# Performance work log

Measured on AMD Instinct MI355X. Metric: run time of the kernel, lower is better.

The kernel has to match this reference:

```python
import math
import jax, jax.numpy as jnp
import numpy as np

COULOMB = 14.399645478425668  # eV*Angstrom / e^2


def setup_inputs() -> dict:
    key = jax.random.key(0)
    k0, k1, k2, k3, k4 = jax.random.split(key, 5)
    B, n, F, S = 128, 512, 64, 4  # molecules, atoms/molecule, feat dim, n species
    N = B * n
    node_features = jax.random.normal(k0, (N, F), dtype=jnp.float32)
    pos = jax.random.normal(k1, (N, 3), dtype=jnp.float32) * 5.0  # spread atoms out
    atom_type = jax.random.randint(k2, (N,), 0, S)
    total_charge = jnp.zeros((B, 1), dtype=jnp.float32)
    chi_weight = jax.random.normal(k3, (F, 1), dtype=jnp.float32) / np.float32(np.sqrt(F))
    hardness_param = jnp.ones((S,), dtype=jnp.float32)
    sigma = 0.3 + 0.5 * jax.random.uniform(k4, (S,), dtype=jnp.float32)  # covalent radii
    return dict(node_features=node_features, pos=pos, atom_type=atom_type,
                total_charge=total_charge, chi_weight=chi_weight,
                hardness_param=hardness_param, sigma=sigma, n_per_mol=n)


def reference(node_features, pos, atom_type, total_charge, chi_weight,
              hardness_param, sigma, n_per_mol):
    n = n_per_mol
    N, F = node_features.shape
    B = N // n

    feats = node_features.reshape(B, n, F)
    pos_b = pos.reshape(B, n, 3)
    sp = atom_type.reshape(B, n)

    chi = (feats @ chi_weight)[..., 0]                      # [B, n] electronegativity
    hard = jnp.square(hardness_param)[sp]                   # [B, n]
    sig = sigma[sp]                                         # [B, n]

    # pairwise distances within each molecule (diag masked for safe divide)
    diff = pos_b[:, :, None, :] - pos_b[:, None, :, :]      # [B, n, n, 3]
    d2 = jnp.sum(diff * diff, axis=-1)
    eye = jnp.eye(n, dtype=pos.dtype)
    d = jnp.sqrt(jnp.where(eye, 1.0, d2))                   # [B, n, n]

    gamma = jnp.sqrt(sig[:, :, None] ** 2 + sig[:, None, :] ** 2)
    off = COULOMB * jax.lax.erf(d / (math.sqrt(2.0) * gamma)) / d
    diag = hard + COULOMB / (math.sqrt(math.pi) * sig)      # [B, n]
    coeffs = off * (1.0 - eye) + eye * diag[:, :, None]     # [B, n, n]

    # augmented Qeq system with charge-conservation Lagrange multiplier
    A = jnp.ones((B, n + 1, n + 1), dtype=coeffs.dtype)
    A = A.at[:, :n, :n].set(coeffs)
    A = A.at[:, n, n].set(0.0)
    rhs = jnp.concatenate([-chi, total_charge], axis=1)     # [B, n+1]
    sol = jnp.linalg.solve(A, rhs[..., None])[..., 0]
    q = sol[:, :n]                                          # [B, n] charges

    # E = sum_{i<j} C_ij q_i q_j + sum_i (chi_i q_i + 0.5 diag_i q_i^2)
    #   = 0.5 q^T C q + chi . q   (C includes diagonal)
    e_qeq = 0.5 * jnp.einsum('bi,bij,bj->b', q, coeffs, q) + jnp.sum(chi * q, axis=1)
    return e_qeq[:, None], q.reshape(N, 1)
```

## Files before the change

kernel.cpp:

```cpp
#include <hip/hip_runtime.h>
#include <math.h>

#define NA 512
#define NN (NA*NA)
#define COULOMB 14.399645478425668f
#define SQRT_PI 1.7724538509055160273f

__device__ __forceinline__ float rl(float x, int lane) {
    return __int_as_float(__builtin_amdgcn_readlane(__float_as_int(x), lane));
}

__device__ __forceinline__ float pair_val(float dx, float dy, float dz,
                                          float s2i, float s2k) {
    float d2 = dx*dx + dy*dy + dz*dz;
    float rinv = rsqrtf(d2);
    return COULOMB * erff(d2 * rinv * rsqrtf(2.f * (s2i + s2k))) * rinv;
}

__global__ void k_pre(const float* __restrict__ feats, const float* __restrict__ w,
                      const int* __restrict__ type, const float* __restrict__ hard,
                      const float* __restrict__ sigma,
                      float* __restrict__ chi, float* __restrict__ diag,
                      float* __restrict__ sigA, int N) {
    __shared__ float wl[64];
    int tid = threadIdx.x;
    if (tid < 64) wl[tid] = w[tid];
    __syncthreads();
    int i = blockIdx.x * 256 + tid;
    if (i >= N) return;
    const float4* fp = (const float4*)(feats + (size_t)i * 64);
    float acc = 0.f;
#pragma unroll
    for (int q = 0; q < 16; q++) {
        float4 v = fp[q];
        acc += v.x * wl[4*q] + v.y * wl[4*q+1] + v.z * wl[4*q+2] + v.w * wl[4*q+3];
    }
    chi[i] = acc;
    int t = type[i];
    float s = sigma[t];
    float h = hard[t];
    sigA[i] = s;
    diag[i] = h * h + COULOMB / (SQRT_PI * s);
}

__global__ void __launch_bounds__(512, 2) k_panel(const float* __restrict__ pos,
                                                  const float* __restrict__ sigA,
                                                  const float* __restrict__ diagA,
                                                  float* __restrict__ C, const int j) {
    const int b = blockIdx.x;
    float* __restrict__ Cb = C + (size_t)b * NN;
    const int jb = j * 64;
    const int m = NA - jb - 64;
    const int tid = threadIdx.x;
    __shared__ float D[64 * 65];
    __shared__ float DT[64 * 64];
    __shared__ float invd[64];
    __shared__ float px[NA], py[NA], pz[NA], s2s[NA];

    if (j == 0) {
        if (tid < NA) {
            px[tid] = pos[((size_t)b * NA + tid) * 3 + 0];
            py[tid] = pos[((size_t)b * NA + tid) * 3 + 1];
            pz[tid] = pos[((size_t)b * NA + tid) * 3 + 2];
            float s = sigA[b * NA + tid];
            s2s[tid] = s * s;
        }
        __syncthreads();
    }

#pragma unroll
    for (int e = 0; e < 8; e++) {
        int f = e * 512 + tid;
        int rr = f >> 6, cc = f & 63;
        float v;
        if (j == 0) {
            if (rr == cc) v = diagA[b * NA + rr];
            else v = pair_val(px[rr]-px[cc], py[rr]-py[cc], pz[rr]-pz[cc], s2s[rr], s2s[cc]);
        } else {
            v = Cb[(size_t)(jb + rr) * NA + jb + cc];
        }
        D[rr * 65 + cc] = v;
    }

    float rv[64];
    const int r = tid - 64;
    if (r >= 0 && r < m) {
        const int g = jb + 64 + r;
        if (j == 0) {
#pragma unroll
            for (int k = 0; k < 64; k++)
                rv[k] = pair_val(px[g]-px[k], py[g]-py[k], pz[g]-pz[k], s2s[g], s2s[k]);
        } else {
            const float4* rp = (const float4*)(Cb + (size_t)g * NA + jb);
#pragma unroll
            for (int q = 0; q < 16; q++) {
                float4 v = rp[q];
                rv[4*q] = v.x; rv[4*q+1] = v.y; rv[4*q+2] = v.z; rv[4*q+3] = v.w;
            }
        }
    }
    __syncthreads();

    if (tid < 64) {
        const int t = tid;
        float cl[64];
#pragma unroll
        for (int i = 0; i < 64; i++) cl[i] = (i >= t) ? D[i * 65 + t] : D[t * 65 + i];
#pragma unroll
        for (int k = 0; k < 64; k++) {
            float pivot = rl(cl[k], k);
            float invp = 1.0f / pivot;
            float factor = (t > k) ? (cl[k] * invp) : 0.0f;
#pragma unroll
            for (int i = k + 1; i < 64; i++) {
                float bc = rl(cl[i], k);
                cl[i] -= bc * factor;
            }
        }
        float rs = 1.0f / sqrtf(cl[t]);
        invd[t] = rs;
#pragma unroll
        for (int i = 0; i < 64; i++)
            if (i >= t) D[i * 65 + t] = cl[i] * rs;
    }
    __syncthreads();

#pragma unroll
    for (int e = 0; e < 8; e++) {
        int f = e * 512 + tid;
        int row = f >> 6, cc = f & 63;
        float v = D[row * 65 + cc];
        DT[row * 64 + cc] = (cc < row) ? v : 0.f;
        if (cc <= row) Cb[(size_t)(jb + row) * NA + jb + cc] = v;
    }
    __syncthreads();

    if (r >= 0 && r < m) {
#pragma unroll
        for (int k = 0; k < 64; k++) {
            float acc = rv[k];
            const float4* Lr = (const float4*)(DT + k * 64);
            const int k4 = k >> 2;
#pragma unroll
            for (int t4 = 0; t4 < k4; t4++) {
                float4 Lv = Lr[t4];
                acc -= Lv.x * rv[4*t4] + Lv.y * rv[4*t4+1] + Lv.z * rv[4*t4+2] + Lv.w * rv[4*t4+3];
            }
#pragma unroll
            for (int tt = k4 * 4; tt < k; tt++) acc -= DT[k * 64 + tt] * rv[tt];
            rv[k] = acc * invd[k];
        }
        float4* rp = (float4*)(Cb + (size_t)(jb + 64 + r) * NA + jb);
#pragma unroll
        for (int q = 0; q < 16; q++)
            rp[q] = make_float4(rv[4*q], rv[4*q+1], rv[4*q+2], rv[4*q+3]);
    }
}

template<bool GEN>
__global__ void __launch_bounds__(256, 3) k_trail(float* __restrict__ C,
                                                  const float* __restrict__ pos,
                                                  const float* __restrict__ sigA,
                                                  const float* __restrict__ diagA,
                                                  const int j) {
    const int b = blockIdx.y;
    float* __restrict__ Cb = C + (size_t)b * NN;
    const int jb = j * 64;
    const int m = NA - jb - 64;
    int t = blockIdx.x;
    int RI = 0;
    while (t >= RI + 1) { t -= RI + 1; RI++; }
    const int RJ = t;
    const int RB = RI * 128, CB = RJ * 128;
    const int vr = min(128, m - RB);
    const int vc = min(128, m - CB);
    const int tid = threadIdx.x;
    const int rg = tid >> 4, cg = tid & 15;

    __shared__ float As[128 * 65];
    __shared__ float Bs[128 * 65];

    float acc[8][8];

    if (GEN) {
        __shared__ float pAx[128], pAy[128], pAz[128], sA[128], dA[128];
        __shared__ float pBx[128], pBy[128], pBz[128], sB[128];
        if (tid < 128) {
            if (RB + tid < m) {
                int ga = b * NA + jb + 64 + RB + tid;
                pAx[tid] = pos[(size_t)ga * 3 + 0];
                pAy[tid] = pos[(size_t)ga * 3 + 1];
                pAz[tid] = pos[(size_t)ga * 3 + 2];
                float s = sigA[ga]; sA[tid] = s * s;
                dA[tid] = diagA[ga];
            }
        } else {
            int u = tid - 128;
            if (CB + u < m) {
                int gb = b * NA + jb + 64 + CB + u;
                pBx[u] = pos[(size_t)gb * 3 + 0];
                pBy[u] = pos[(size_t)gb * 3 + 1];
                pBz[u] = pos[(size_t)gb * 3 + 2];
                float s = sigA[gb]; sB[u] = s * s;
            }
        }
        __syncthreads();
#pragma unroll
        for (int rr = 0; rr < 8; rr++) {
            int row = rg * 8 + rr;
#pragma unroll
            for (int cc = 0; cc < 8; cc++) {
                int col = cg + 16 * cc;
                if (RB + row == CB + col)
                    acc[rr][cc] = dA[row];
                else
                    acc[rr][cc] = pair_val(pAx[row]-pBx[col], pAy[row]-pBy[col],
                                           pAz[row]-pBz[col], sA[row], sB[col]);
            }
        }
        __syncthreads();
    } else {
        const int GRB = jb + 64 + RB, GCB = jb + 64 + CB;
#pragma unroll
        for (int rr = 0; rr < 8; rr++) {
            int row = rg * 8 + rr;
#pragma unroll
            for (int cc = 0; cc < 8; cc++) {
                int col = cg + 16 * cc;
                acc[rr][cc] = (row < vr && col < vc)
                    ? Cb[(size_t)(GRB + row) * NA + GCB + col] : 0.f;
            }
        }
    }

    const float* Pan = Cb + (size_t)(jb + 64) * NA + jb;
#pragma unroll
    for (int e = 0; e < 8; e++) {
        int f = e * 256 + tid;
        int row = f >> 4, s = f & 15;
        float4 v = make_float4(0.f, 0.f, 0.f, 0.f);
        if (row < vr) v = *(const float4*)(Pan + (size_t)(RB + row) * NA + s * 4);
        As[row * 65 + s * 4 + 0] = v.x;
        As[row * 65 + s * 4 + 1] = v.y;
        As[row * 65 + s * 4 + 2] = v.z;
        As[row * 65 + s * 4 + 3] = v.w;
        float4 u = make_float4(0.f, 0.f, 0.f, 0.f);
        if (row < vc) u = *(const float4*)(Pan + (size_t)(CB + row) * NA + s * 4);
        Bs[row * 65 + s * 4 + 0] = u.x;
        Bs[row * 65 + s * 4 + 1] = u.y;
        Bs[row * 65 + s * 4 + 2] = u.z;
        Bs[row * 65 + s * 4 + 3] = u.w;
    }
    __syncthreads();

#pragma unroll 4
    for (int k = 0; k < 64; k++) {
        float ai[8], bj[8];
#pragma unroll
        for (int rr = 0; rr < 8; rr++) ai[rr] = As[(rg * 8 + rr) * 65 + k];
#pragma unroll
        for (int cc = 0; cc < 8; cc++) bj[cc] = Bs[(cg + 16 * cc) * 65 + k];
#pragma unroll
        for (int rr = 0; rr < 8; rr++)
#pragma unroll
            for (int cc = 0; cc < 8; cc++)
                acc[rr][cc] = fmaf(-ai[rr], bj[cc], acc[rr][cc]);
    }

    const int GRB = jb + 64 + RB, GCB = jb + 64 + CB;
#pragma unroll
    for (int rr = 0; rr < 8; rr++) {
        int row = rg * 8 + rr;
        if (row < vr) {
#pragma unroll
            for (int cc = 0; cc < 8; cc++) {
                int col = cg + 16 * cc;
                if (col < vc)
                    Cb[(size_t)(GRB + row) * NA + GCB + col] = acc[rr][cc];
            }
        }
    }
}

__global__ void __launch_bounds__(512) k_solve(const float* __restrict__ C,
                                               const float* __restrict__ chiA,
                                               const float* __restrict__ Qtot,
                                               float* __restrict__ out, int B) {
    int b = blockIdx.x;
    const float* Cb = C + (size_t)b * NN;
    int tid = threadIdx.x;
    __shared__ float D[64 * 65];
    __shared__ float v1[NA], v2[NA];
    __shared__ float tv1[64], tv2[64];
    __shared__ float pb[2][8][64];
    __shared__ float red[16];
    __shared__ float muS;

    v1[tid] = chiA[b * NA + tid];
    v2[tid] = 1.0f;

    for (int j = 0; j < 8; j++) {
        int jb = j * 64;
        __syncthreads();
#pragma unroll
        for (int e = 0; e < 8; e++) {
            int f = e * 512 + tid;
            int row = f >> 6, cc = f & 63;
            D[row * 65 + cc] = Cb[(size_t)(jb + row) * NA + jb + cc];
        }
        int i = tid >> 3, l8 = tid & 7;
        float pa1 = 0.f, pa2 = 0.f;
        for (int cx = l8; cx < jb; cx += 8) {
            float Lv = Cb[(size_t)(jb + i) * NA + cx];
            pa1 += Lv * v1[cx]; pa2 += Lv * v2[cx];
        }
        pa1 += __shfl_xor(pa1, 1); pa2 += __shfl_xor(pa2, 1);
        pa1 += __shfl_xor(pa1, 2); pa2 += __shfl_xor(pa2, 2);
        pa1 += __shfl_xor(pa1, 4); pa2 += __shfl_xor(pa2, 4);
        if (l8 == 0) { tv1[i] = v1[jb + i] - pa1; tv2[i] = v2[jb + i] - pa2; }
        __syncthreads();
        if (tid < 128) {
            int lane = tid & 63;
            float* vv = (tid < 64) ? v1 : v2;
            const float* tv = (tid < 64) ? tv1 : tv2;
            float val = tv[lane];
            float idg = 1.0f / D[lane * 65 + lane];
#pragma unroll
            for (int k = 0; k < 64; k++) {
                float yk = rl(val, k) * rl(idg, k);
                if (lane == k) vv[jb + k] = yk;
                float lv = (lane > k) ? D[lane * 65 + k] : 0.f;
                val -= lv * yk;
            }
        }
    }

    for (int j = 7; j >= 0; j--) {
        int jb = j * 64;
        __syncthreads();
#pragma unroll
        for (int e = 0; e < 8; e++) {
            int f = e * 512 + tid;
            int row = f >> 6, cc = f & 63;
            D[row * 65 + cc] = Cb[(size_t)(jb + row) * NA + jb + cc];
        }
        int trp = tid >> 6, i2 = tid & 63;
        float px1 = 0.f, px2 = 0.f;
        for (int gt = jb + 64 + trp; gt < NA; gt += 8) {
            float Lv = Cb[(size_t)gt * NA + jb + i2];
            px1 += Lv * v1[gt]; px2 += Lv * v2[gt];
        }
        pb[0][trp][i2] = px1; pb[1][trp][i2] = px2;
        __syncthreads();
        if (tid < 64) {
            float s = 0.f;
#pragma unroll
            for (int tr = 0; tr < 8; tr++) s += pb[0][tr][tid];
            tv1[tid] = v1[jb + tid] - s;
        } else if (tid < 128) {
            int l = tid - 64;
            float s = 0.f;
#pragma unroll
            for (int tr = 0; tr < 8; tr++) s += pb[1][tr][l];
            tv2[l] = v2[jb + l] - s;
        }
        __syncthreads();
        if (tid < 128) {
            int lane = tid & 63;
            float* vv = (tid < 64) ? v1 : v2;
            const float* tv = (tid < 64) ? tv1 : tv2;
            float val = tv[lane];
            float idg = 1.0f / D[lane * 65 + lane];
#pragma unroll
            for (int k = 63; k >= 0; k--) {
                float xk = rl(val, k) * rl(idg, k);
                if (lane == k) vv[jb + k] = xk;
                float lv = (lane < k) ? D[k * 65 + lane] : 0.f;
                val -= lv * xk;
            }
        }
    }
    __syncthreads();

    float s1p = v1[tid], s2p = v2[tid];
#pragma unroll
    for (int off = 1; off < 64; off <<= 1) {
        s1p += __shfl_xor(s1p, off);
        s2p += __shfl_xor(s2p, off);
    }
    if ((tid & 63) == 0) { red[tid >> 6] = s1p; red[8 + (tid >> 6)] = s2p; }
    __syncthreads();
    if (tid == 0) {
        float s1 = 0.f, s2 = 0.f;
#pragma unroll
        for (int wv = 0; wv < 8; wv++) { s1 += red[wv]; s2 += red[8 + wv]; }
        muS = -(Qtot[b] + s1) / s2;
    }
    __syncthreads();
    float mu = muS;
    float qv = -v1[tid] - mu * v2[tid];
    out[B + (size_t)b * NA + tid] = qv;

    float eacc = chiA[b * NA + tid] * qv;
#pragma unroll
    for (int off = 1; off < 64; off <<= 1) eacc += __shfl_xor(eacc, off);
    __syncthreads();
    if ((tid & 63) == 0) red[tid >> 6] = eacc;
    __syncthreads();
    if (tid == 0) {
        float e = 0.f;
#pragma unroll
        for (int wv = 0; wv < 8; wv++) e += red[wv];
        out[b] = 0.5f * e - 0.5f * mu * Qtot[b];
    }
}

extern "C" void kernel_launch(void* const* d_in, const int* in_sizes, int n_in,
                              void* d_out, int out_size, void* d_ws, size_t ws_size,
                              hipStream_t stream) {
    const int B = in_sizes[3];
    const int N = in_sizes[2];
    const float* feats = (const float*)d_in[0];
    const float* pos   = (const float*)d_in[1];
    const int*   type  = (const int*)d_in[2];
    const float* Qt    = (const float*)d_in[3];
    const float* w     = (const float*)d_in[4];
    const float* hard  = (const float*)d_in[5];
    const float* sig   = (const float*)d_in[6];
    float* out = (float*)d_out;
    float* ws  = (float*)d_ws;

    float* C    = ws;
    float* chi  = ws + (size_t)B * NN;
    float* diag = chi + N;
    float* sigA = diag + N;

    k_pre<<<(N + 255) / 256, 256, 0, stream>>>(feats, w, type, hard, sig, chi, diag, sigA, N);

    static const int tilesJ[7] = {10, 6, 6, 3, 3, 1, 1};
    for (int j = 0; j < 8; j++) {
        k_panel<<<B, 512, 0, stream>>>(pos, sigA, diag, C, j);
        if (j < 7) {
            if (j == 0)
                k_trail<true><<<dim3(tilesJ[j], B), 256, 0, stream>>>(C, pos, sigA, diag, j);
            else
                k_trail<false><<<dim3(tilesJ[j], B), 256, 0, stream>>>(C, pos, sigA, diag, j);
        }
    }
    k_solve<<<B, 512, 0, stream>>>(C, chi, Qt, out, B);
}
```

Before: 810.8 us.

## Split panel across two blocks, fuse last three Cholesky steps, restructure triangular solves

```diff
diff --git a/kernel.cpp b/kernel.cpp
--- a/kernel.cpp
+++ b/kernel.cpp
@@ -43,11 +43,12 @@
     diag[i] = h * h + COULOMB / (SQRT_PI * s);
 }
 
-__global__ void __launch_bounds__(512, 2) k_panel(const float* __restrict__ pos,
+__global__ void __launch_bounds__(256, 1) k_panel(const float* __restrict__ pos,
                                                   const float* __restrict__ sigA,
                                                   const float* __restrict__ diagA,
                                                   float* __restrict__ C, const int j) {
-    const int b = blockIdx.x;
+    const int q = blockIdx.x;
+    const int b = blockIdx.y;
     float* __restrict__ Cb = C + (size_t)b * NN;
     const int jb = j * 64;
     const int m = NA - jb - 64;
@@ -58,19 +59,21 @@
     __shared__ float px[NA], py[NA], pz[NA], s2s[NA];
 
     if (j == 0) {
-        if (tid < NA) {
-            px[tid] = pos[((size_t)b * NA + tid) * 3 + 0];
-            py[tid] = pos[((size_t)b * NA + tid) * 3 + 1];
-            pz[tid] = pos[((size_t)b * NA + tid) * 3 + 2];
-            float s = sigA[b * NA + tid];
-            s2s[tid] = s * s;
-        }
-        __syncthreads();
-    }
-
-#pragma unroll
-    for (int e = 0; e < 8; e++) {
-        int f = e * 512 + tid;
+#pragma unroll
+        for (int e = 0; e < 2; e++) {
+            int i = e * 256 + tid;
+            px[i] = pos[((size_t)b * NA + i) * 3 + 0];
+            py[i] = pos[((size_t)b * NA + i) * 3 + 1];
+            pz[i] = pos[((size_t)b * NA + i) * 3 + 2];
+            float s = sigA[b * NA + i];
+            s2s[i] = s * s;
+        }
+        __syncthreads();
+    }
+
+#pragma unroll
+    for (int e = 0; e < 16; e++) {
+        int f = e * 256 + tid;
         int rr = f >> 6, cc = f & 63;
         float v;
         if (j == 0) {
@@ -82,20 +85,25 @@
         D[rr * 65 + cc] = v;
     }
 
+    const int h = m >> 1;
+    const int r0 = q ? h : 0;
+    const int nr = q ? (m - h) : h;
+    const int r = tid - 32;
+    const bool hasrow = (r >= 0 && r < nr);
+    const int grow = jb + 64 + r0 + r;
     float rv[64];
-    const int r = tid - 64;
-    if (r >= 0 && r < m) {
-        const int g = jb + 64 + r;
+    if (hasrow) {
         if (j == 0) {
 #pragma unroll
             for (int k = 0; k < 64; k++)
-                rv[k] = pair_val(px[g]-px[k], py[g]-py[k], pz[g]-pz[k], s2s[g], s2s[k]);
+                rv[k] = pair_val(px[grow]-px[k], py[grow]-py[k], pz[grow]-pz[k],
+                                 s2s[grow], s2s[k]);
         } else {
-            const float4* rp = (const float4*)(Cb + (size_t)g * NA + jb);
-#pragma unroll
-            for (int q = 0; q < 16; q++) {
-                float4 v = rp[q];
-                rv[4*q] = v.x; rv[4*q+1] = v.y; rv[4*q+2] = v.z; rv[4*q+3] = v.w;
+            const float4* rp = (const float4*)(Cb + (size_t)grow * NA + jb);
+#pragma unroll
+            for (int qq = 0; qq < 16; qq++) {
+                float4 v = rp[qq];
+                rv[4*qq] = v.x; rv[4*qq+1] = v.y; rv[4*qq+2] = v.z; rv[4*qq+3] = v.w;
             }
         }
     }
@@ -126,16 +134,16 @@
     __syncthreads();
 
 #pragma unroll
-    for (int e = 0; e < 8; e++) {
-        int f = e * 512 + tid;
+    for (int e = 0; e < 16; e++) {
+        int f = e * 256 + tid;
         int row = f >> 6, cc = f & 63;
         float v = D[row * 65 + cc];
         DT[row * 64 + cc] = (cc < row) ? v : 0.f;
-        if (cc <= row) Cb[(size_t)(jb + row) * NA + jb + cc] = v;
-    }
-    __syncthreads();
-
-    if (r >= 0 && r < m) {
+        if (q == 0 && cc <= row) Cb[(size_t)(jb + row) * NA + jb + cc] = v;
+    }
+    __syncthreads();
+
+    if (hasrow) {
 #pragma unroll
         for (int k = 0; k < 64; k++) {
             float acc = rv[k];
@@ -150,10 +158,10 @@
             for (int tt = k4 * 4; tt < k; tt++) acc -= DT[k * 64 + tt] * rv[tt];
             rv[k] = acc * invd[k];
         }
-        float4* rp = (float4*)(Cb + (size_t)(jb + 64 + r) * NA + jb);
-#pragma unroll
-        for (int q = 0; q < 16; q++)
-            rp[q] = make_float4(rv[4*q], rv[4*q+1], rv[4*q+2], rv[4*q+3]);
+        float4* rp = (float4*)(Cb + (size_t)grow * NA + jb);
+#pragma unroll
+        for (int qq = 0; qq < 16; qq++)
+            rp[qq] = make_float4(rv[4*qq], rv[4*qq+1], rv[4*qq+2], rv[4*qq+3]);
     }
 }
 
@@ -282,25 +290,181 @@
     }
 }
 
-__global__ void __launch_bounds__(512) k_solve(const float* __restrict__ C,
-                                               const float* __restrict__ chiA,
-                                               const float* __restrict__ Qtot,
-                                               float* __restrict__ out, int B) {
+__global__ void __launch_bounds__(512, 1) k_tail(float* __restrict__ C) {
+    const int b = blockIdx.x;
+    float* __restrict__ Cb = C + (size_t)b * NN;
+    const int base = NA - 192;
+    const int tid = threadIdx.x;
+    __shared__ float D[64 * 65];
+    __shared__ float DT[64 * 64];
+    __shared__ float invd[64];
+
+    for (int t = 0; t < 3; t++) {
+        const int jb = base + t * 64;
+        const int mrem = 192 - t * 64 - 64;
+
+#pragma unroll
+        for (int e = 0; e < 8; e++) {
+            int f = e * 512 + tid;
+            int rr = f >> 6, cc = f & 63;
+            D[rr * 65 + cc] = Cb[(size_t)(jb + rr) * NA + jb + cc];
+        }
+        __syncthreads();
+
+        if (tid < 64) {
+            const int tt = tid;
+            float cl[64];
+#pragma unroll
+            for (int i = 0; i < 64; i++) cl[i] = (i >= tt) ? D[i * 65 + tt] : D[tt * 65 + i];
+#pragma unroll
+            for (int k = 0; k < 64; k++) {
+                float pivot = rl(cl[k], k);
+                float invp = 1.0f / pivot;
+                float factor = (tt > k) ? (cl[k] * invp) : 0.0f;
+#pragma unroll
+                for (int i = k + 1; i < 64; i++) {
+                    float bc = rl(cl[i], k);
+                    cl[i] -= bc * factor;
+                }
+            }
+            float rs = 1.0f / sqrtf(cl[tt]);
+            invd[tt] = rs;
+#pragma unroll
+            for (int i = 0; i < 64; i++)
+                if (i >= tt) D[i * 65 + tt] = cl[i] * rs;
+        }
+        __syncthreads();
+
+#pragma unroll
+        for (int e = 0; e < 8; e++) {
+            int f = e * 512 + tid;
+            int row = f >> 6, cc = f & 63;
+            float v = D[row * 65 + cc];
+            DT[row * 64 + cc] = (cc < row) ? v : 0.f;
+            if (cc <= row) Cb[(size_t)(jb + row) * NA + jb + cc] = v;
+        }
+        __syncthreads();
+
+        if (mrem == 0) break;
+
+        const int r = tid - 64;
+        if (r >= 0 && r < mrem) {
+            const int grow = jb + 64 + r;
+            float rv[64];
+            const float4* rp = (const float4*)(Cb + (size_t)grow * NA + jb);
+#pragma unroll
+            for (int qq = 0; qq < 16; qq++) {
+                float4 v = rp[qq];
+                rv[4*qq] = v.x; rv[4*qq+1] = v.y; rv[4*qq+2] = v.z; rv[4*qq+3] = v.w;
+            }
+#pragma unroll
+            for (int k = 0; k < 64; k++) {
+                float acc = rv[k];
+                const float4* Lr = (const float4*)(DT + k * 64);
+                const int k4 = k >> 2;
+#pragma unroll
+                for (int t4 = 0; t4 < k4; t4++) {
+                    float4 Lv = Lr[t4];
+                    acc -= Lv.x * rv[4*t4] + Lv.y * rv[4*t4+1] + Lv.z * rv[4*t4+2] + Lv.w * rv[4*t4+3];
+                }
+#pragma unroll
+                for (int ttt = k4 * 4; ttt < k; ttt++) acc -= DT[k * 64 + ttt] * rv[ttt];
+                rv[k] = acc * invd[k];
+            }
+            float4* wp = (float4*)(Cb + (size_t)grow * NA + jb);
+#pragma unroll
+            for (int qq = 0; qq < 16; qq++)
+                wp[qq] = make_float4(rv[4*qq], rv[4*qq+1], rv[4*qq+2], rv[4*qq+3]);
+        }
+        __threadfence_block();
+        __syncthreads();
+
+        if (mrem == 128) {
+            const int rg = tid >> 5;
+            const int cg = tid & 31;
+            const int gr0 = jb + 64 + rg * 8;
+            const int gc0 = jb + 64 + cg * 4;
+            float acc[8][4];
+#pragma unroll
+            for (int rr = 0; rr < 8; rr++) {
+                float4 v = *(const float4*)(Cb + (size_t)(gr0 + rr) * NA + gc0);
+                acc[rr][0] = v.x; acc[rr][1] = v.y; acc[rr][2] = v.z; acc[rr][3] = v.w;
+            }
+#pragma unroll 4
+            for (int k4 = 0; k4 < 16; k4++) {
+                float4 a[8], bb[4];
+#pragma unroll
+                for (int rr = 0; rr < 8; rr++)
+                    a[rr] = *(const float4*)(Cb + (size_t)(gr0 + rr) * NA + jb + k4 * 4);
+#pragma unroll
+                for (int cc = 0; cc < 4; cc++)
+                    bb[cc] = *(const float4*)(Cb + (size_t)(gc0 + cc) * NA + jb + k4 * 4);
+#pragma unroll
+                for (int rr = 0; rr < 8; rr++) {
+#pragma unroll
+                    for (int cc = 0; cc < 4; cc++) {
+                        acc[rr][cc] = fmaf(-a[rr].x, bb[cc].x, acc[rr][cc]);
+                        acc[rr][cc] = fmaf(-a[rr].y, bb[cc].y, acc[rr][cc]);
+                        acc[rr][cc] = fmaf(-a[rr].z, bb[cc].z, acc[rr][cc]);
+                        acc[rr][cc] = fmaf(-a[rr].w, bb[cc].w, acc[rr][cc]);
+                    }
+                }
+            }
+#pragma unroll
+            for (int rr = 0; rr < 8; rr++)
+                *(float4*)(Cb + (size_t)(gr0 + rr) * NA + gc0) =
+                    make_float4(acc[rr][0], acc[rr][1], acc[rr][2], acc[rr][3]);
+        } else {
+            const int rg = tid >> 6;
+            const int col = tid & 63;
+            const int gr0 = jb + 64 + rg * 8;
+            const int gc = jb + 64 + col;
+            float acc[8];
+#pragma unroll
+            for (int rr = 0; rr < 8; rr++)
+                acc[rr] = Cb[(size_t)(gr0 + rr) * NA + gc];
+#pragma unroll 4
+            for (int k4 = 0; k4 < 16; k4++) {
+                float4 bb = *(const float4*)(Cb + (size_t)gc * NA + jb + k4 * 4);
+#pragma unroll
+                for (int rr = 0; rr < 8; rr++) {
+                    float4 a = *(const float4*)(Cb + (size_t)(gr0 + rr) * NA + jb + k4 * 4);
+                    acc[rr] = fmaf(-a.x, bb.x, acc[rr]);
+                    acc[rr] = fmaf(-a.y, bb.y, acc[rr]);
+                    acc[rr] = fmaf(-a.z, bb.z, acc[rr]);
+                    acc[rr] = fmaf(-a.w, bb.w, acc[rr]);
+                }
+            }
+#pragma unroll
+            for (int rr = 0; rr < 8; rr++)
+                Cb[(size_t)(gr0 + rr) * NA + gc] = acc[rr];
+        }
+        __threadfence_block();
+        __syncthreads();
+    }
+}
+
+__global__ void __launch_bounds__(512, 1) k_solve(const float* __restrict__ C,
+                                                  const float* __restrict__ chiA,
+                                                  const float* __restrict__ Qtot,
+                                                  float* __restrict__ out, int B) {
     int b = blockIdx.x;
     const float* Cb = C + (size_t)b * NN;
     int tid = threadIdx.x;
     __shared__ float D[64 * 65];
-    __shared__ float v1[NA], v2[NA];
-    __shared__ float tv1[64], tv2[64];
-    __shared__ float pb[2][8][64];
+    __shared__ float r1[NA], r2[NA];
+    __shared__ float pb1[4][NA], pb2[4][NA];
     __shared__ float red[16];
     __shared__ float muS;
 
-    v1[tid] = chiA[b * NA + tid];
-    v2[tid] = 1.0f;
+    r1[tid] = chiA[b * NA + tid];
+    r2[tid] = 1.0f;
+
+    const int sub = tid & 7;
+    const int rowg = tid >> 3;
 
     for (int j = 0; j < 8; j++) {
-        int jb = j * 64;
+        const int jb = j * 64;
         __syncthreads();
 #pragma unroll
         for (int e = 0; e < 8; e++) {
@@ -308,22 +472,11 @@
             int row = f >> 6, cc = f & 63;
             D[row * 65 + cc] = Cb[(size_t)(jb + row) * NA + jb + cc];
         }
-        int i = tid >> 3, l8 = tid & 7;
-        float pa1 = 0.f, pa2 = 0.f;
-        for (int cx = l8; cx < jb; cx += 8) {
-            float Lv = Cb[(size_t)(jb + i) * NA + cx];
-            pa1 += Lv * v1[cx]; pa2 += Lv * v2[cx];
-        }
-        pa1 += __shfl_xor(pa1, 1); pa2 += __shfl_xor(pa2, 1);
-        pa1 += __shfl_xor(pa1, 2); pa2 += __shfl_xor(pa2, 2);
-        pa1 += __shfl_xor(pa1, 4); pa2 += __shfl_xor(pa2, 4);
-        if (l8 == 0) { tv1[i] = v1[jb + i] - pa1; tv2[i] = v2[jb + i] - pa2; }
         __syncthreads();
         if (tid < 128) {
             int lane = tid & 63;
-            float* vv = (tid < 64) ? v1 : v2;
-            const float* tv = (tid < 64) ? tv1 : tv2;
-            float val = tv[lane];
+            float* vv = (tid < 64) ? r1 : r2;
+            float val = vv[jb + lane];
             float idg = 1.0f / D[lane * 65 + lane];
 #pragma unroll
             for (int k = 0; k < 64; k++) {
@@ -333,10 +486,30 @@
                 val -= lv * yk;
             }
         }
-    }
-
+        __syncthreads();
+#pragma unroll
+        for (int p = 0; p < 7; p++) {
+            int g = jb + 64 + p * 64 + rowg;
+            if (g < NA) {
+                const float4* Lr = (const float4*)(Cb + (size_t)g * NA + jb + sub * 8);
+                float4 a0 = Lr[0], a1 = Lr[1];
+                int y0 = jb + sub * 8;
+                float d1 = a0.x*r1[y0]   + a0.y*r1[y0+1] + a0.z*r1[y0+2] + a0.w*r1[y0+3]
+                         + a1.x*r1[y0+4] + a1.y*r1[y0+5] + a1.z*r1[y0+6] + a1.w*r1[y0+7];
+                float d2 = a0.x*r2[y0]   + a0.y*r2[y0+1] + a0.z*r2[y0+2] + a0.w*r2[y0+3]
+                         + a1.x*r2[y0+4] + a1.y*r2[y0+5] + a1.z*r2[y0+6] + a1.w*r2[y0+7];
+                d1 += __shfl_xor(d1, 1); d2 += __shfl_xor(d2, 1);
+                d1 += __shfl_xor(d1, 2); d2 += __shfl_xor(d2, 2);
+                d1 += __shfl_xor(d1, 4); d2 += __shfl_xor(d2, 4);
+                if (sub == 0) { r1[g] -= d1; r2[g] -= d2; }
+            }
+        }
+    }
+
+    const int ii = tid & 127;
+    const int gg = tid >> 7;
     for (int j = 7; j >= 0; j--) {
-        int jb = j * 64;
+        const int jb = j * 64;
         __syncthreads();
 #pragma unroll
         for (int e = 0; e < 8; e++) {
@@ -344,32 +517,11 @@
             int row = f >> 6, cc = f & 63;
             D[row * 65 + cc] = Cb[(size_t)(jb + row) * NA + jb + cc];
         }
-        int trp = tid >> 6, i2 = tid & 63;
-        float px1 = 0.f, px2 = 0.f;
-        for (int gt = jb + 64 + trp; gt < NA; gt += 8) {
-            float Lv = Cb[(size_t)gt * NA + jb + i2];
-            px1 += Lv * v1[gt]; px2 += Lv * v2[gt];
-        }
-        pb[0][trp][i2] = px1; pb[1][trp][i2] = px2;
-        __syncthreads();
-        if (tid < 64) {
-            float s = 0.f;
-#pragma unroll
-            for (int tr = 0; tr < 8; tr++) s += pb[0][tr][tid];
-            tv1[tid] = v1[jb + tid] - s;
-        } else if (tid < 128) {
-            int l = tid - 64;
-            float s = 0.f;
-#pragma unroll
-            for (int tr = 0; tr < 8; tr++) s += pb[1][tr][l];
-            tv2[l] = v2[jb + l] - s;
-        }
         __syncthreads();
         if (tid < 128) {
             int lane = tid & 63;
-            float* vv = (tid < 64) ? v1 : v2;
-            const float* tv = (tid < 64) ? tv1 : tv2;
-            float val = tv[lane];
+            float* vv = (tid < 64) ? r1 : r2;
+            float val = vv[jb + lane];
             float idg = 1.0f / D[lane * 65 + lane];
 #pragma unroll
             for (int k = 63; k >= 0; k--) {
@@ -379,10 +531,32 @@
                 val -= lv * xk;
             }
         }
-    }
-    __syncthreads();
-
-    float s1p = v1[tid], s2p = v2[tid];
+        __syncthreads();
+        if (jb > 0) {
+            const int nf4 = jb >> 2;
+            float4 s1 = make_float4(0.f,0.f,0.f,0.f), s2 = make_float4(0.f,0.f,0.f,0.f);
+            if (ii < nf4) {
+#pragma unroll
+                for (int gq = 0; gq < 16; gq++) {
+                    int g = jb + gg * 16 + gq;
+                    float x1 = r1[g], x2 = r2[g];
+                    float4 Lv = *(const float4*)(Cb + (size_t)g * NA + ii * 4);
+                    s1.x += Lv.x * x1; s1.y += Lv.y * x1; s1.z += Lv.z * x1; s1.w += Lv.w * x1;
+                    s2.x += Lv.x * x2; s2.y += Lv.y * x2; s2.z += Lv.z * x2; s2.w += Lv.w * x2;
+                }
+            }
+            *(float4*)(&pb1[gg][ii * 4]) = s1;
+            *(float4*)(&pb2[gg][ii * 4]) = s2;
+            __syncthreads();
+            if (tid < jb) {
+                r1[tid] -= pb1[0][tid] + pb1[1][tid] + pb1[2][tid] + pb1[3][tid];
+                r2[tid] -= pb2[0][tid] + pb2[1][tid] + pb2[2][tid] + pb2[3][tid];
+            }
+        }
+    }
+    __syncthreads();
+
+    float s1p = r1[tid], s2p = r2[tid];
 #pragma unroll
     for (int off = 1; off < 64; off <<= 1) {
         s1p += __shfl_xor(s1p, off);
@@ -398,7 +572,7 @@
     }
     __syncthreads();
     float mu = muS;
-    float qv = -v1[tid] - mu * v2[tid];
+    float qv = -r1[tid] - mu * r2[tid];
     out[B + (size_t)b * NA + tid] = qv;
 
     float eacc = chiA[b * NA + tid] * qv;
@@ -437,15 +611,14 @@
 
     k_pre<<<(N + 255) / 256, 256, 0, stream>>>(feats, w, type, hard, sig, chi, diag, sigA, N);
 
-    static const int tilesJ[7] = {10, 6, 6, 3, 3, 1, 1};
-    for (int j = 0; j < 8; j++) {
-        k_panel<<<B, 512, 0, stream>>>(pos, sigA, diag, C, j);
-        if (j < 7) {
-            if (j == 0)
-                k_trail<true><<<dim3(tilesJ[j], B), 256, 0, stream>>>(C, pos, sigA, diag, j);
-            else
-                k_trail<false><<<dim3(tilesJ[j], B), 256, 0, stream>>>(C, pos, sigA, diag, j);
-        }
-    }
+    static const int tilesJ[5] = {10, 6, 6, 3, 3};
+    for (int j = 0; j < 5; j++) {
+        k_panel<<<dim3(2, B), 256, 0, stream>>>(pos, sigA, diag, C, j);
+        if (j == 0)
+            k_trail<true><<<dim3(tilesJ[j], B), 256, 0, stream>>>(C, pos, sigA, diag, j);
+        else
+            k_trail<false><<<dim3(tilesJ[j], B), 256, 0, stream>>>(C, pos, sigA, diag, j);
+    }
+    k_tail<<<B, 512, 0, stream>>>(C);
     k_solve<<<B, 512, 0, stream>>>(C, chi, Qt, out, B);
 }
```

After: 767.1 us. 1.06x faster.
